# Performance work log

Measured on AMD Instinct MI355X. Metric: run time of the kernel, lower is better.

Reference implementation:

```python
import jax, jax.numpy as jnp
import numpy as np

B, S, E, H = 4, 2048, 512, 8
D = E // H  # head dim
CDIM = 3


def setup_inputs() -> dict:
    key = jax.random.key(0)
    ks = jax.random.split(key, 16)
    inp = {
        'q': jax.random.normal(ks[0], (B, S, E), jnp.float32),
        'k': jax.random.normal(ks[1], (B, S, E), jnp.float32),
        'v': jax.random.normal(ks[2], (B, S, E), jnp.float32),
        'coords_q': jax.random.normal(ks[3], (B, S, CDIM), jnp.float32),
        'coords_k': jax.random.normal(ks[4], (B, S, CDIM), jnp.float32),
        'attn_mask': jax.random.randint(ks[5], (B, S, S), 0, 2).astype(bool),
        'alibi_mask': jax.random.randint(ks[6], (B, S, S), 0, 2).astype(bool),
        # per-head projection params, stacked over heads: [H, E, D]
        'Wq': jax.random.normal(ks[7], (H, E, D), jnp.float32) / np.sqrt(E),
        'bq': jnp.zeros((H, D), jnp.float32),
        'Wk': jax.random.normal(ks[8], (H, E, D), jnp.float32) / np.sqrt(E),
        'bk': jnp.zeros((H, D), jnp.float32),
        'Wv': jax.random.normal(ks[9], (H, E, D), jnp.float32) / np.sqrt(E),
        'bv': jnp.zeros((H, D), jnp.float32),
        # per-head ALiBi params; running_mean is a buffer (eval mode -> constant ones)
        'bias_scale': jax.random.uniform(ks[10], (H,), jnp.float32),
        'running_mean': jnp.ones((H,), jnp.float32),
        # output projection
        'fc_w': jax.random.normal(ks[11], (E, E), jnp.float32) / np.sqrt(E),
        'fc_b': jnp.zeros((E,), jnp.float32),
    }
    return inp


def reference(q, k, v, coords_q, coords_k, attn_mask, alibi_mask,
              Wq, bq, Wk, bk, Wv, bv, bias_scale, running_mean, fc_w, fc_b):
    # per-head projections, vectorized over heads: [B,H,S,D]
    qh = jnp.einsum('bse,hed->bhsd', q, Wq) + bq[None, :, None, :]
    kh = jnp.einsum('bse,hed->bhsd', k, Wk) + bk[None, :, None, :]
    vh = jnp.einsum('bse,hed->bhsd', v, Wv) + bv[None, :, None, :]

    # scaled dot-product logits: [B,H,Sq,Sk]
    logits = jnp.einsum('bhqd,bhkd->bhqk', qh, kh) * (D ** -0.5)
    weights = jax.nn.softmax(logits, axis=-1)

    # pairwise euclidean distances between coords: [B,Sq,Sk]
    diff = coords_q[:, :, None, :] - coords_k[:, None, :, :]
    dist = jnp.sqrt(jnp.sum(diff * diff, axis=-1))

    # per-head distance bias (eval: divide by running_mean buffer, scale by bias_scale)
    scale = (bias_scale / running_mean)[None, :, None, None]  # [1,H,1,1]
    scaled_dist = dist[:, None, :, :] * scale                  # [B,H,Sq,Sk]
    masked_dist = jnp.where(~alibi_mask[:, None, :, :], scaled_dist, 0.0)

    # post-softmax bias subtraction and masking (non-standard attention)
    masked = jnp.where(~attn_mask[:, None, :, :], weights - masked_dist, 0.0)

    att = jnp.einsum('bhqk,bhkd->bhqd', masked, vh)            # [B,H,S,D]
    att = att.transpose(0, 2, 1, 3).reshape(B, S, E)           # [B,S,E]
    return att @ fc_w.T + fc_b
```

## Files before the change

### kernel.cpp

```cpp
#include <hip/hip_runtime.h>

typedef unsigned short ushort;
typedef unsigned char uchar;
typedef unsigned long long u64;
typedef __attribute__((ext_vector_type(8))) short short8;
typedef __attribute__((ext_vector_type(4))) float f32x4;
typedef __attribute__((ext_vector_type(4))) unsigned int uint4v;

#define B_ 4
#define S_ 2048
#define E_ 512
#define H_ 8
#define D_ 64
#define LDT 40
#define LDF 68

__device__ inline ushort f2bf(float f) {
  union { float f; unsigned int u; } v; v.f = f;
  unsigned int u = v.u;
  unsigned int r = u + 0x7FFFu + ((u >> 16) & 1u);
  return (ushort)(r >> 16);
}

__device__ inline unsigned int cvt_pk_bf16(float a, float b) {
  unsigned int r;
  asm("v_cvt_pk_bf16_f32 %0, %1, %2" : "=v"(r) : "v"(a), "v"(b));
  return r;
}

__device__ inline float exp2_fast(float x) {
#if defined(__has_builtin)
#if __has_builtin(__builtin_amdgcn_exp2f)
  return __builtin_amdgcn_exp2f(x);
#else
  return __expf(x * 0.69314718056f);
#endif
#else
  return __expf(x * 0.69314718056f);
#endif
}

__device__ inline short8 mask_keep(short8 p, short8 a2) {
  union U { short8 s; uint4v u; } P, A;
  P.s = p; A.s = a2;
#pragma unroll
  for (int i = 0; i < 4; ++i) {
    unsigned int t = A.u[i] & 0x80008000u;
    unsigned int dm = (t >> 15) * 0xFFFFu;
    P.u[i] &= ~dm;
  }
  return P.s;
}

__device__ inline float dpp_sum16(float v) {
  union { float f; int i; } s, t;
  s.f = v;
  t.i = __builtin_amdgcn_update_dpp(0, s.i, 0x128, 0xf, 0xf, false); s.f += t.f;
  t.i = __builtin_amdgcn_update_dpp(0, s.i, 0x124, 0xf, 0xf, false); s.f += t.f;
  t.i = __builtin_amdgcn_update_dpp(0, s.i, 0x122, 0xf, 0xf, false); s.f += t.f;
  t.i = __builtin_amdgcn_update_dpp(0, s.i, 0x121, 0xf, 0xf, false); s.f += t.f;
  return s.f;
}

__global__ void detect_kernel(const uchar* __restrict__ am, int* flag) {
  __shared__ int s;
  if (threadIdx.x == 0) s = 0;
  __syncthreads();
  int x = 0;
  for (int p = threadIdx.x; p < 4096; p += 256)
    if (p & 3) x += am[p];
  atomicAdd(&s, x);
  __syncthreads();
  if (threadIdx.x == 0) *flag = (s == 0) ? 1 : 0;
}

__global__ __launch_bounds__(256) void convert_w_kernel(
    const float* __restrict__ Wq, const float* __restrict__ Wk, const float* __restrict__ Wv,
    ushort* __restrict__ wt) {
  const int p = blockIdx.y;
  const float* W = (p == 0) ? Wq : (p == 1) ? Wk : Wv;
  const int n = blockIdx.x;
  const int h = n >> 6, d = n & 63;
  ushort* o = wt + ((size_t)p * E_ + n) * E_;
  for (int e = threadIdx.x; e < E_; e += 256)
    o[e] = f2bf(W[((size_t)h * E_ + e) * D_ + d]);
}

__global__ __launch_bounds__(256) void convert_fcw_kernel(
    const float* __restrict__ fcw, ushort* __restrict__ fcwbf) {
  size_t base = ((size_t)blockIdx.x * 256 + threadIdx.x) * 8;
  float4 a = *(const float4*)&fcw[base];
  float4 b = *(const float4*)&fcw[base + 4];
  short8 o;
  o[0] = (short)f2bf(a.x); o[1] = (short)f2bf(a.y); o[2] = (short)f2bf(a.z); o[3] = (short)f2bf(a.w);
  o[4] = (short)f2bf(b.x); o[5] = (short)f2bf(b.y); o[6] = (short)f2bf(b.z); o[7] = (short)f2bf(b.w);
  *(short8*)&fcwbf[base] = o;
}

__global__ __launch_bounds__(256) void proj_gemm_kernel(
    const float* __restrict__ qx, const float* __restrict__ kx, const float* __restrict__ vx,
    const ushort* __restrict__ wt,
    const float* __restrict__ bq, const float* __restrict__ bk, const float* __restrict__ bv,
    ushort* __restrict__ qkv) {
  const int phys = blockIdx.x;
  const int logical = (phys & 7) * 96 + (phys >> 3);
  const int p = logical >> 8;
  const int rem = logical & 255;
  const int m0 = (rem >> 2) * 128, n0 = (rem & 3) * 128;

  const float* A   = (p == 0) ? qx : (p == 1) ? kx : vx;
  const ushort* Bt = wt + (size_t)p * (E_ * E_);
  const float* bias = (p == 0) ? bq : (p == 1) ? bk : bv;
  const float osc = (p == 0) ? 0.125f * 1.44269504f : 1.0f;
  ushort* out = qkv + (size_t)p * (B_ * H_ * S_ * D_);

  const int tid = threadIdx.x;
  const int w = tid >> 6, lane = tid & 63;
  const int g = lane >> 4, c = lane & 15;
  const int wr = w >> 1, wc = w & 1;

  __shared__ ushort As[128][LDT], Bs[128][LDT];

  f32x4 acc[4][4];
#pragma unroll
  for (int i = 0; i < 4; ++i)
#pragma unroll
    for (int j = 0; j < 4; ++j) acc[i][j] = (f32x4){0, 0, 0, 0};

  const int srow = tid >> 2, sc8 = (tid & 3) * 8;
  float4 pa0[2], pa1[2];
  short8 pb[2];
#pragma unroll
  for (int it = 0; it < 2; ++it) {
    const float* ap = &A[(size_t)(m0 + srow + 64 * it) * E_ + sc8];
    pa0[it] = *(const float4*)ap;
    pa1[it] = *(const float4*)(ap + 4);
    pb[it] = *(const short8*)&Bt[(size_t)(n0 + srow + 64 * it) * E_ + sc8];
  }

  for (int kk = 0; kk < E_; kk += 32) {
    __syncthreads();
#pragma unroll
    for (int it = 0; it < 2; ++it) {
      unsigned int r0 = cvt_pk_bf16(pa0[it].x, pa0[it].y), r1 = cvt_pk_bf16(pa0[it].z, pa0[it].w);
      unsigned int r2 = cvt_pk_bf16(pa1[it].x, pa1[it].y), r3 = cvt_pk_bf16(pa1[it].z, pa1[it].w);
      short8 av;
      av[0] = (short)(ushort)r0; av[1] = (short)(ushort)(r0 >> 16);
      av[2] = (short)(ushort)r1; av[3] = (short)(ushort)(r1 >> 16);
      av[4] = (short)(ushort)r2; av[5] = (short)(ushort)(r2 >> 16);
      av[6] = (short)(ushort)r3; av[7] = (short)(ushort)(r3 >> 16);
      *(short8*)&As[srow + 64 * it][sc8] = av;
      *(short8*)&Bs[srow + 64 * it][sc8] = pb[it];
    }
    __syncthreads();
    if (kk + 32 < E_) {
#pragma unroll
      for (int it = 0; it < 2; ++it) {
        const float* ap = &A[(size_t)(m0 + srow + 64 * it) * E_ + kk + 32 + sc8];
        pa0[it] = *(const float4*)ap;
        pa1[it] = *(const float4*)(ap + 4);
        pb[it] = *(const short8*)&Bt[(size_t)(n0 + srow + 64 * it) * E_ + kk + 32 + sc8];
      }
    }
    short8 af[4], bfr[4];
#pragma unroll
    for (int i = 0; i < 4; ++i) af[i] = *(const short8*)&As[wr * 64 + i * 16 + c][8 * g];
#pragma unroll
    for (int j = 0; j < 4; ++j) bfr[j] = *(const short8*)&Bs[wc * 64 + j * 16 + c][8 * g];
#pragma unroll
    for (int i = 0; i < 4; ++i)
#pragma unroll
      for (int j = 0; j < 4; ++j)
        acc[i][j] = __builtin_amdgcn_mfma_f32_16x16x32_bf16(af[i], bfr[j], acc[i][j], 0, 0, 0);
  }

#pragma unroll
  for (int i = 0; i < 4; ++i)
#pragma unroll
    for (int jj = 0; jj < 4; ++jj) {
      int grow = m0 + wr * 64 + i * 16 + 4 * g + jj;
      int b = grow >> 11, s = grow & 2047;
#pragma unroll
      for (int j = 0; j < 4; ++j) {
        int col = n0 + wc * 64 + j * 16 + c;
        int h = col >> 6, d = col & 63;
        out[(((size_t)(b * H_ + h)) * S_ + s) * D_ + d] = f2bf((acc[i][j][jj] + bias[col]) * osc);
      }
    }
}

__global__ __launch_bounds__(256) void transpose_v_kernel(
    const ushort* __restrict__ vh, ushort* __restrict__ vtg) {
  const int bh = blockIdx.y, s0 = blockIdx.x * 64;
  __shared__ ushort tile[64][70];
  const int tid = threadIdx.x;
#pragma unroll
  for (int it = 0; it < 2; ++it) {
    int chunk = tid + 256 * it;
    int r = chunk >> 3, c8 = chunk & 7;
    *(short8*)&tile[r][c8 * 8] = *(const short8*)&vh[((size_t)bh * S_ + s0 + r) * D_ + c8 * 8];
  }
  __syncthreads();
#pragma unroll
  for (int it = 0; it < 2; ++it) {
    int chunk = tid + 256 * it;
    int d = chunk >> 3, s8 = chunk & 7;
    short8 o;
#pragma unroll
    for (int j = 0; j < 8; ++j) o[j] = (short)tile[s8 * 8 + j][d];
    *(short8*)&vtg[((size_t)bh * D_ + d) * S_ + s0 + s8 * 8] = o;
  }
}

__global__ __launch_bounds__(256) void m2dist_kernel(
    const float* __restrict__ cq, const float* __restrict__ ck,
    const void* __restrict__ am_raw, const void* __restrict__ alm_raw,
    const int* __restrict__ flag,
    ushort* __restrict__ m2d) {
  const bool isInt = (*flag != 0);
  const int b = blockIdx.y, qi = blockIdx.x;
  const int k0 = threadIdx.x * 8;
  const size_t rowbase = ((size_t)b * S_ + qi) * S_;
  const float qx = cq[((size_t)b * S_ + qi) * 3 + 0];
  const float qy = cq[((size_t)b * S_ + qi) * 3 + 1];
  const float qz = cq[((size_t)b * S_ + qi) * 3 + 2];
  int a[8], al[8];
  if (isInt) {
    int4 A0 = *(const int4*)&((const int*)am_raw)[rowbase + k0];
    int4 A1 = *(const int4*)&((const int*)am_raw)[rowbase + k0 + 4];
    int4 L0 = *(const int4*)&((const int*)alm_raw)[rowbase + k0];
    int4 L1 = *(const int4*)&((const int*)alm_raw)[rowbase + k0 + 4];
    a[0]=A0.x; a[1]=A0.y; a[2]=A0.z; a[3]=A0.w; a[4]=A1.x; a[5]=A1.y; a[6]=A1.z; a[7]=A1.w;
    al[0]=L0.x; al[1]=L0.y; al[2]=L0.z; al[3]=L0.w; al[4]=L1.x; al[5]=L1.y; al[6]=L1.z; al[7]=L1.w;
  } else {
    u64 ab = *(const u64*)&((const uchar*)am_raw)[rowbase + k0];
    u64 lb = *(const u64*)&((const uchar*)alm_raw)[rowbase + k0];
#pragma unroll
    for (int j = 0; j < 8; ++j) { a[j] = (int)((ab >> (8 * j)) & 0xFF); al[j] = (int)((lb >> (8 * j)) & 0xFF); }
  }
  float c24[24];
  {
    const float* ckp = ck + ((size_t)b * S_ + k0) * 3;
#pragma unroll
    for (int t = 0; t < 6; ++t) {
      float4 cv = *(const float4*)(ckp + 4 * t);
      c24[4 * t] = cv.x; c24[4 * t + 1] = cv.y; c24[4 * t + 2] = cv.z; c24[4 * t + 3] = cv.w;
    }
  }
  float dist[8];
#pragma unroll
  for (int j = 0; j < 8; ++j) {
    const float dx = qx - c24[3 * j], dy = qy - c24[3 * j + 1], dz = qz - c24[3 * j + 2];
    dist[j] = sqrtf(dx * dx + dy * dy + dz * dz);
  }
  short8 md;
#pragma unroll
  for (int jp = 0; jp < 4; ++jp) {
    unsigned int r = cvt_pk_bf16(dist[2 * jp], dist[2 * jp + 1]);
    ushort v0 = (!a[2 * jp]     && !al[2 * jp])     ? (ushort)r         : (ushort)0;
    ushort v1 = (!a[2 * jp + 1] && !al[2 * jp + 1]) ? (ushort)(r >> 16) : (ushort)0;
    if (a[2 * jp])     v0 |= 0x8000u;
    if (a[2 * jp + 1]) v1 |= 0x8000u;
    md[2 * jp] = (short)v0; md[2 * jp + 1] = (short)v1;
  }
  *(short8*)&m2d[rowbase + k0] = md;
}

__global__ __launch_bounds__(512) void flash_kernel(
    const ushort* __restrict__ qh, const ushort* __restrict__ kh, const ushort* __restrict__ vtg,
    const ushort* __restrict__ m2d,
    const float* __restrict__ bscale, const float* __restrict__ rmean,
    ushort* __restrict__ attb) {
  const int flat = blockIdx.x;
  const int h = flat >> 6;
  const int grp = flat & 63;
  const int b = grp >> 4;
  const int qb = (grp & 15) * 128;
  const int bh = b * 8 + h;
  const int tid = threadIdx.x;
  const int w = tid >> 6, lane = tid & 63;
  const int g = lane >> 4, c = lane & 15;

  __shared__ ushort Kt[2][64][LDF];
  __shared__ ushort Vt[2][64][LDF];
  __shared__ ushort Pl[8][16][LDF];

  const size_t bhS = (size_t)bh * S_;
  const int qrow_a = qb + 16 * w + c;
  const short8 aq0 = *(const short8*)(qh + (bhS + qrow_a) * D_ + 8 * g);
  const short8 aq1 = *(const short8*)(qh + (bhS + qrow_a) * D_ + 8 * g + 32);

  const int skr = tid >> 3, sc8 = (tid & 7) * 8;
  const ushort* pk0 = kh + (bhS + skr) * D_ + sc8;
  const ushort* pv0 = vtg + ((size_t)bh * D_ + skr) * S_ + sc8;
  const ushort* pm0 = m2d + ((size_t)b * S_ + qrow_a) * S_ + 8 * g;
  const ushort* pm1 = pm0 + 32;

  f32x4 acc1[4], acc2[4];
#pragma unroll
  for (int t = 0; t < 4; ++t) { acc1[t] = (f32x4){0,0,0,0}; acc2[t] = (f32x4){0,0,0,0}; }
  float l[4] = {0, 0, 0, 0};

  {
    short8 k0 = *(const short8*)pk0;  pk0 += 64 * D_;
    short8 v0 = *(const short8*)pv0;  pv0 += 64;
    *(short8*)&Kt[0][skr][sc8] = k0;
    *(short8*)&Vt[0][skr][sc8] = v0;
  }
  short8 a2n0 = *(const short8*)pm0; pm0 += 64;
  short8 a2n1 = *(const short8*)pm1; pm1 += 64;
  short8 skn = *(const short8*)pk0;  pk0 += 64 * D_;
  short8 svn = *(const short8*)pv0;  pv0 += 64;
  __syncthreads();

  for (int kb = 0; kb < S_; kb += 64) {
    const int cur = (kb >> 6) & 1;
    short8 a2c0 = a2n0, a2c1 = a2n1;
    a2n0 = *(const short8*)pm0; pm0 += 64;
    a2n1 = *(const short8*)pm1; pm1 += 64;

    f32x4 sf[4];
    __builtin_amdgcn_s_setprio(1);
#pragma unroll
    for (int t = 0; t < 4; ++t) {
      short8 b0 = *(const short8*)&Kt[cur][16 * t + c][8 * g];
      short8 b1 = *(const short8*)&Kt[cur][16 * t + c][8 * g + 32];
      f32x4 z = (f32x4){0, 0, 0, 0};
      z = __builtin_amdgcn_mfma_f32_16x16x32_bf16(aq0, b0, z, 0, 0, 0);
      z = __builtin_amdgcn_mfma_f32_16x16x32_bf16(aq1, b1, z, 0, 0, 0);
      sf[t] = z;
    }
    __builtin_amdgcn_s_setprio(0);

#pragma unroll
    for (int t = 0; t < 4; ++t)
#pragma unroll
      for (int jp = 0; jp < 2; ++jp) {
        float p0 = exp2_fast(sf[t][2 * jp]);
        float p1 = exp2_fast(sf[t][2 * jp + 1]);
        l[2 * jp] += p0; l[2 * jp + 1] += p1;
        unsigned int r = cvt_pk_bf16(p0, p1);
        Pl[w][4 * g + 2 * jp][16 * t + c]     = (ushort)r;
        Pl[w][4 * g + 2 * jp + 1][16 * t + c] = (ushort)(r >> 16);
      }

    asm volatile("s_waitcnt lgkmcnt(0)" ::: "memory");
    __builtin_amdgcn_sched_barrier(0);

    short8 pa0 = *(const short8*)&Pl[w][c][8 * g];
    short8 pa1 = *(const short8*)&Pl[w][c][8 * g + 32];
    pa0 = mask_keep(pa0, a2c0);
    pa1 = mask_keep(pa1, a2c1);
    __builtin_amdgcn_s_setprio(1);
#pragma unroll
    for (int t2 = 0; t2 < 4; ++t2) {
      short8 v0 = *(const short8*)&Vt[cur][16 * t2 + c][8 * g];
      short8 v1 = *(const short8*)&Vt[cur][16 * t2 + c][8 * g + 32];
      acc1[t2] = __builtin_amdgcn_mfma_f32_16x16x32_bf16(pa0, v0, acc1[t2], 0, 0, 0);
      acc1[t2] = __builtin_amdgcn_mfma_f32_16x16x32_bf16(pa1, v1, acc1[t2], 0, 0, 0);
      acc2[t2] = __builtin_amdgcn_mfma_f32_16x16x32_bf16(a2c0, v0, acc2[t2], 0, 0, 0);
      acc2[t2] = __builtin_amdgcn_mfma_f32_16x16x32_bf16(a2c1, v1, acc2[t2], 0, 0, 0);
    }
    __builtin_amdgcn_s_setprio(0);

    if (kb + 64 < S_) {
      *(short8*)&Kt[cur ^ 1][skr][sc8] = skn;
      *(short8*)&Vt[cur ^ 1][skr][sc8] = svn;
      skn = *(const short8*)pk0;  pk0 += 64 * D_;
      svn = *(const short8*)pv0;  pv0 += 64;
    }
    __syncthreads();
  }

  float linv[4];
#pragma unroll
  for (int j = 0; j < 4; ++j) linv[j] = 1.0f / dpp_sum16(l[j]);
  const float scale = bscale[h] / rmean[h];
#pragma unroll
  for (int t2 = 0; t2 < 4; ++t2)
#pragma unroll
    for (int j = 0; j < 4; ++j) {
      int qr = qb + 16 * w + 4 * g + j;
      int d = 16 * t2 + c;
      attb[(((size_t)b * S_ + qr) * H_ + h) * D_ + d] =
          f2bf(acc1[t2][j] * linv[j] - scale * acc2[t2][j]);
    }
}

__global__ __launch_bounds__(256) void final_gemm_kernel(
    const ushort* __restrict__ attb, const ushort* __restrict__ fcwbf,
    const float* __restrict__ fcb, float* __restrict__ out) {
  const int phys = blockIdx.x;
  const int logical = (phys & 7) * 32 + (phys >> 3);
  const int m0 = (logical >> 2) * 128, n0 = (logical & 3) * 128;
  const int tid = threadIdx.x;
  const int w = tid >> 6, lane = tid & 63;
  const int g = lane >> 4, c = lane & 15;
  const int wr = w >> 1, wc = w & 1;

  __shared__ ushort As[128][LDT], Bs[128][LDT];

  f32x4 acc[4][4];
#pragma unroll
  for (int i = 0; i < 4; ++i)
#pragma unroll
    for (int j = 0; j < 4; ++j) acc[i][j] = (f32x4){0, 0, 0, 0};

  const int srow = tid >> 2, sc8 = (tid & 3) * 8;
  short8 pa[2], pb[2];
#pragma unroll
  for (int it = 0; it < 2; ++it) {
    pa[it] = *(const short8*)&attb[(size_t)(m0 + srow + 64 * it) * E_ + sc8];
    pb[it] = *(const short8*)&fcwbf[(size_t)(n0 + srow + 64 * it) * E_ + sc8];
  }

  for (int kk = 0; kk < E_; kk += 32) {
    __syncthreads();
#pragma unroll
    for (int it = 0; it < 2; ++it) {
      *(short8*)&As[srow + 64 * it][sc8] = pa[it];
      *(short8*)&Bs[srow + 64 * it][sc8] = pb[it];
    }
    __syncthreads();
    if (kk + 32 < E_) {
#pragma unroll
      for (int it = 0; it < 2; ++it) {
        pa[it] = *(const short8*)&attb[(size_t)(m0 + srow + 64 * it) * E_ + kk + 32 + sc8];
        pb[it] = *(const short8*)&fcwbf[(size_t)(n0 + srow + 64 * it) * E_ + kk + 32 + sc8];
      }
    }
    short8 af[4], bfr[4];
#pragma unroll
    for (int i = 0; i < 4; ++i) af[i] = *(const short8*)&As[wr * 64 + i * 16 + c][8 * g];
#pragma unroll
    for (int j = 0; j < 4; ++j) bfr[j] = *(const short8*)&Bs[wc * 64 + j * 16 + c][8 * g];
#pragma unroll
    for (int i = 0; i < 4; ++i)
#pragma unroll
      for (int j = 0; j < 4; ++j)
        acc[i][j] = __builtin_amdgcn_mfma_f32_16x16x32_bf16(af[i], bfr[j], acc[i][j], 0, 0, 0);
  }

#pragma unroll
  for (int i = 0; i < 4; ++i)
#pragma unroll
    for (int jj = 0; jj < 4; ++jj) {
      int grow = m0 + wr * 64 + i * 16 + 4 * g + jj;
#pragma unroll
      for (int j = 0; j < 4; ++j) {
        int col = n0 + wc * 64 + j * 16 + c;
        out[(size_t)grow * E_ + col] = acc[i][j][jj] + fcb[col];
      }
    }
}

extern "C" void kernel_launch(void* const* d_in, const int* in_sizes, int n_in,
                              void* d_out, int out_size, void* d_ws, size_t ws_size,
                              hipStream_t stream) {
  const float* q   = (const float*)d_in[0];
  const float* k   = (const float*)d_in[1];
  const float* v   = (const float*)d_in[2];
  const float* cq  = (const float*)d_in[3];
  const float* ck  = (const float*)d_in[4];
  const void*  am  = d_in[5];
  const void*  alm = d_in[6];
  const float* Wq  = (const float*)d_in[7];
  const float* bq  = (const float*)d_in[8];
  const float* Wk  = (const float*)d_in[9];
  const float* bk  = (const float*)d_in[10];
  const float* Wv  = (const float*)d_in[11];
  const float* bv  = (const float*)d_in[12];
  const float* bsc = (const float*)d_in[13];
  const float* rm  = (const float*)d_in[14];
  const float* fcw = (const float*)d_in[15];
  const float* fcb = (const float*)d_in[16];
  float* out = (float*)d_out;

  char* ws = (char*)d_ws;
  ushort* attb = (ushort*)(ws);
  ushort* vtg  = (ushort*)(ws + 16ull * 1024 * 1024);
  ushort* qkv  = (ushort*)(ws + 24ull * 1024 * 1024);
  ushort* m2d  = (ushort*)(ws + 48ull * 1024 * 1024);
  ushort* wt   = (ushort*)(ws + 80ull * 1024 * 1024);
  ushort* fcwbf= (ushort*)(ws + 80ull * 1024 * 1024 + 1536 * 1024);
  int*    flag = (int*)   (ws + 82ull * 1024 * 1024);

  ushort* qh = qkv;
  ushort* kh = qkv + (size_t)(B_ * H_ * S_ * D_);
  ushort* vh = qkv + 2 * (size_t)(B_ * H_ * S_ * D_);

  detect_kernel<<<1, 256, 0, stream>>>((const uchar*)am, flag);
  convert_w_kernel<<<dim3(512, 3), 256, 0, stream>>>(Wq, Wk, Wv, wt);
  convert_fcw_kernel<<<128, 256, 0, stream>>>(fcw, fcwbf);
  proj_gemm_kernel<<<768, 256, 0, stream>>>(q, k, v, wt, bq, bk, bv, qkv);
  transpose_v_kernel<<<dim3(S_ / 64, B_ * H_), 256, 0, stream>>>(vh, vtg);
  m2dist_kernel<<<dim3(S_, B_), 256, 0, stream>>>(cq, ck, am, alm, flag, m2d);
  flash_kernel<<<512, 512, 0, stream>>>(qh, kh, vtg, m2d, bsc, rm, attb);
  final_gemm_kernel<<<256, 256, 0, stream>>>(attb, fcwbf, fcb, out);
}
```

Measured before the change: 171.2 us.

## Have each flash-attention wave process two 16-row query groups with 256 threads

The flash kernel now runs 4 waves per block instead of 8. Each wave handles two 16-row query tiles and reuses the same K and V fragments read from LDS for both, which halves LDS reads of K/V per unit of work. Each thread also stages two rows of K and V per tile. This costs more registers per wave (double accumulators, extra mask prefetches) and fewer waves per block to hide latency.

```diff
diff --git a/kernel.cpp b/kernel.cpp
--- a/kernel.cpp
+++ b/kernel.cpp
@@ -266,7 +266,7 @@
   *(short8*)&m2d[rowbase + k0] = md;
 }
 
-__global__ __launch_bounds__(512) void flash_kernel(
+__global__ __launch_bounds__(256) void flash_kernel(
     const ushort* __restrict__ qh, const ushort* __restrict__ kh, const ushort* __restrict__ vtg,
     const ushort* __restrict__ m2d,
     const float* __restrict__ bscale, const float* __restrict__ rmean,
@@ -283,52 +283,68 @@
 
   __shared__ ushort Kt[2][64][LDF];
   __shared__ ushort Vt[2][64][LDF];
-  __shared__ ushort Pl[8][16][LDF];
+  __shared__ ushort Pl[4][32][LDF];
 
   const size_t bhS = (size_t)bh * S_;
-  const int qrow_a = qb + 16 * w + c;
-  const short8 aq0 = *(const short8*)(qh + (bhS + qrow_a) * D_ + 8 * g);
-  const short8 aq1 = *(const short8*)(qh + (bhS + qrow_a) * D_ + 8 * g + 32);
+  const int qr0 = qb + 16 * w + c;
+  const int qr1 = qr0 + 64;
+  const short8 aq0 = *(const short8*)(qh + (bhS + qr0) * D_ + 8 * g);
+  const short8 aq1 = *(const short8*)(qh + (bhS + qr0) * D_ + 8 * g + 32);
+  const short8 aq2 = *(const short8*)(qh + (bhS + qr1) * D_ + 8 * g);
+  const short8 aq3 = *(const short8*)(qh + (bhS + qr1) * D_ + 8 * g + 32);
 
   const int skr = tid >> 3, sc8 = (tid & 7) * 8;
   const ushort* pk0 = kh + (bhS + skr) * D_ + sc8;
+  const ushort* pk1 = pk0 + 32 * D_;
   const ushort* pv0 = vtg + ((size_t)bh * D_ + skr) * S_ + sc8;
-  const ushort* pm0 = m2d + ((size_t)b * S_ + qrow_a) * S_ + 8 * g;
+  const ushort* pv1 = pv0 + 32 * S_;
+  const ushort* pm0 = m2d + ((size_t)b * S_ + qr0) * S_ + 8 * g;
   const ushort* pm1 = pm0 + 32;
-
-  f32x4 acc1[4], acc2[4];
-#pragma unroll
-  for (int t = 0; t < 4; ++t) { acc1[t] = (f32x4){0,0,0,0}; acc2[t] = (f32x4){0,0,0,0}; }
-  float l[4] = {0, 0, 0, 0};
-
-  {
-    short8 k0 = *(const short8*)pk0;  pk0 += 64 * D_;
-    short8 v0 = *(const short8*)pv0;  pv0 += 64;
-    *(short8*)&Kt[0][skr][sc8] = k0;
-    *(short8*)&Vt[0][skr][sc8] = v0;
-  }
+  const ushort* pm2 = m2d + ((size_t)b * S_ + qr1) * S_ + 8 * g;
+  const ushort* pm3 = pm2 + 32;
+
+  f32x4 acc1g0[4], acc2g0[4], acc1g1[4], acc2g1[4];
+#pragma unroll
+  for (int t = 0; t < 4; ++t) {
+    acc1g0[t] = (f32x4){0,0,0,0}; acc2g0[t] = (f32x4){0,0,0,0};
+    acc1g1[t] = (f32x4){0,0,0,0}; acc2g1[t] = (f32x4){0,0,0,0};
+  }
+  float l0[4] = {0, 0, 0, 0}, l1[4] = {0, 0, 0, 0};
+
+  *(short8*)&Kt[0][skr][sc8]      = *(const short8*)pk0;  pk0 += 64 * D_;
+  *(short8*)&Kt[0][skr + 32][sc8] = *(const short8*)pk1;  pk1 += 64 * D_;
+  *(short8*)&Vt[0][skr][sc8]      = *(const short8*)pv0;  pv0 += 64;
+  *(short8*)&Vt[0][skr + 32][sc8] = *(const short8*)pv1;  pv1 += 64;
   short8 a2n0 = *(const short8*)pm0; pm0 += 64;
   short8 a2n1 = *(const short8*)pm1; pm1 += 64;
-  short8 skn = *(const short8*)pk0;  pk0 += 64 * D_;
-  short8 svn = *(const short8*)pv0;  pv0 += 64;
+  short8 a2n2 = *(const short8*)pm2; pm2 += 64;
+  short8 a2n3 = *(const short8*)pm3; pm3 += 64;
+  short8 skn0 = *(const short8*)pk0;  pk0 += 64 * D_;
+  short8 skn1 = *(const short8*)pk1;  pk1 += 64 * D_;
+  short8 svn0 = *(const short8*)pv0;  pv0 += 64;
+  short8 svn1 = *(const short8*)pv1;  pv1 += 64;
   __syncthreads();
 
   for (int kb = 0; kb < S_; kb += 64) {
     const int cur = (kb >> 6) & 1;
-    short8 a2c0 = a2n0, a2c1 = a2n1;
+    short8 a2c0 = a2n0, a2c1 = a2n1, a2c2 = a2n2, a2c3 = a2n3;
     a2n0 = *(const short8*)pm0; pm0 += 64;
     a2n1 = *(const short8*)pm1; pm1 += 64;
-
-    f32x4 sf[4];
+    a2n2 = *(const short8*)pm2; pm2 += 64;
+    a2n3 = *(const short8*)pm3; pm3 += 64;
+
+    f32x4 sf0[4], sf1[4];
     __builtin_amdgcn_s_setprio(1);
 #pragma unroll
     for (int t = 0; t < 4; ++t) {
       short8 b0 = *(const short8*)&Kt[cur][16 * t + c][8 * g];
       short8 b1 = *(const short8*)&Kt[cur][16 * t + c][8 * g + 32];
-      f32x4 z = (f32x4){0, 0, 0, 0};
-      z = __builtin_amdgcn_mfma_f32_16x16x32_bf16(aq0, b0, z, 0, 0, 0);
-      z = __builtin_amdgcn_mfma_f32_16x16x32_bf16(aq1, b1, z, 0, 0, 0);
-      sf[t] = z;
+      f32x4 z0 = (f32x4){0, 0, 0, 0}, z1 = (f32x4){0, 0, 0, 0};
+      z0 = __builtin_amdgcn_mfma_f32_16x16x32_bf16(aq0, b0, z0, 0, 0, 0);
+      z0 = __builtin_amdgcn_mfma_f32_16x16x32_bf16(aq1, b1, z0, 0, 0, 0);
+      z1 = __builtin_amdgcn_mfma_f32_16x16x32_bf16(aq2, b0, z1, 0, 0, 0);
+      z1 = __builtin_amdgcn_mfma_f32_16x16x32_bf16(aq3, b1, z1, 0, 0, 0);
+      sf0[t] = z0; sf1[t] = z1;
     }
     __builtin_amdgcn_s_setprio(0);
 
@@ -336,12 +352,18 @@
     for (int t = 0; t < 4; ++t)
 #pragma unroll
       for (int jp = 0; jp < 2; ++jp) {
-        float p0 = exp2_fast(sf[t][2 * jp]);
-        float p1 = exp2_fast(sf[t][2 * jp + 1]);
-        l[2 * jp] += p0; l[2 * jp + 1] += p1;
+        float p0 = exp2_fast(sf0[t][2 * jp]);
+        float p1 = exp2_fast(sf0[t][2 * jp + 1]);
+        l0[2 * jp] += p0; l0[2 * jp + 1] += p1;
         unsigned int r = cvt_pk_bf16(p0, p1);
         Pl[w][4 * g + 2 * jp][16 * t + c]     = (ushort)r;
         Pl[w][4 * g + 2 * jp + 1][16 * t + c] = (ushort)(r >> 16);
+        float p2 = exp2_fast(sf1[t][2 * jp]);
+        float p3 = exp2_fast(sf1[t][2 * jp + 1]);
+        l1[2 * jp] += p2; l1[2 * jp + 1] += p3;
+        unsigned int r2 = cvt_pk_bf16(p2, p3);
+        Pl[w][16 + 4 * g + 2 * jp][16 * t + c]     = (ushort)r2;
+        Pl[w][16 + 4 * g + 2 * jp + 1][16 * t + c] = (ushort)(r2 >> 16);
       }
 
     asm volatile("s_waitcnt lgkmcnt(0)" ::: "memory");
@@ -349,41 +371,58 @@
 
     short8 pa0 = *(const short8*)&Pl[w][c][8 * g];
     short8 pa1 = *(const short8*)&Pl[w][c][8 * g + 32];
+    short8 pa2 = *(const short8*)&Pl[w][16 + c][8 * g];
+    short8 pa3 = *(const short8*)&Pl[w][16 + c][8 * g + 32];
     pa0 = mask_keep(pa0, a2c0);
     pa1 = mask_keep(pa1, a2c1);
+    pa2 = mask_keep(pa2, a2c2);
+    pa3 = mask_keep(pa3, a2c3);
     __builtin_amdgcn_s_setprio(1);
 #pragma unroll
     for (int t2 = 0; t2 < 4; ++t2) {
       short8 v0 = *(const short8*)&Vt[cur][16 * t2 + c][8 * g];
       short8 v1 = *(const short8*)&Vt[cur][16 * t2 + c][8 * g + 32];
-      acc1[t2] = __builtin_amdgcn_mfma_f32_16x16x32_bf16(pa0, v0, acc1[t2], 0, 0, 0);
-      acc1[t2] = __builtin_amdgcn_mfma_f32_16x16x32_bf16(pa1, v1, acc1[t2], 0, 0, 0);
-      acc2[t2] = __builtin_amdgcn_mfma_f32_16x16x32_bf16(a2c0, v0, acc2[t2], 0, 0, 0);
-      acc2[t2] = __builtin_amdgcn_mfma_f32_16x16x32_bf16(a2c1, v1, acc2[t2], 0, 0, 0);
+      acc1g0[t2] = __builtin_amdgcn_mfma_f32_16x16x32_bf16(pa0, v0, acc1g0[t2], 0, 0, 0);
+      acc1g0[t2] = __builtin_amdgcn_mfma_f32_16x16x32_bf16(pa1, v1, acc1g0[t2], 0, 0, 0);
+      acc2g0[t2] = __builtin_amdgcn_mfma_f32_16x16x32_bf16(a2c0, v0, acc2g0[t2], 0, 0, 0);
+      acc2g0[t2] = __builtin_amdgcn_mfma_f32_16x16x32_bf16(a2c1, v1, acc2g0[t2], 0, 0, 0);
+      acc1g1[t2] = __builtin_amdgcn_mfma_f32_16x16x32_bf16(pa2, v0, acc1g1[t2], 0, 0, 0);
+      acc1g1[t2] = __builtin_amdgcn_mfma_f32_16x16x32_bf16(pa3, v1, acc1g1[t2], 0, 0, 0);
+      acc2g1[t2] = __builtin_amdgcn_mfma_f32_16x16x32_bf16(a2c2, v0, acc2g1[t2], 0, 0, 0);
+      acc2g1[t2] = __builtin_amdgcn_mfma_f32_16x16x32_bf16(a2c3, v1, acc2g1[t2], 0, 0, 0);
     }
     __builtin_amdgcn_s_setprio(0);
 
     if (kb + 64 < S_) {
-      *(short8*)&Kt[cur ^ 1][skr][sc8] = skn;
-      *(short8*)&Vt[cur ^ 1][skr][sc8] = svn;
-      skn = *(const short8*)pk0;  pk0 += 64 * D_;
-      svn = *(const short8*)pv0;  pv0 += 64;
+      *(short8*)&Kt[cur ^ 1][skr][sc8]      = skn0;
+      *(short8*)&Kt[cur ^ 1][skr + 32][sc8] = skn1;
+      *(short8*)&Vt[cur ^ 1][skr][sc8]      = svn0;
+      *(short8*)&Vt[cur ^ 1][skr + 32][sc8] = svn1;
+      skn0 = *(const short8*)pk0;  pk0 += 64 * D_;
+      skn1 = *(const short8*)pk1;  pk1 += 64 * D_;
+      svn0 = *(const short8*)pv0;  pv0 += 64;
+      svn1 = *(const short8*)pv1;  pv1 += 64;
     }
     __syncthreads();
   }
 
-  float linv[4];
-#pragma unroll
-  for (int j = 0; j < 4; ++j) linv[j] = 1.0f / dpp_sum16(l[j]);
+  float linv0[4], linv1[4];
+#pragma unroll
+  for (int j = 0; j < 4; ++j) {
+    linv0[j] = 1.0f / dpp_sum16(l0[j]);
+    linv1[j] = 1.0f / dpp_sum16(l1[j]);
+  }
   const float scale = bscale[h] / rmean[h];
 #pragma unroll
   for (int t2 = 0; t2 < 4; ++t2)
 #pragma unroll
     for (int j = 0; j < 4; ++j) {
-      int qr = qb + 16 * w + 4 * g + j;
+      int qrA = qb + 16 * w + 4 * g + j;
       int d = 16 * t2 + c;
-      attb[(((size_t)b * S_ + qr) * H_ + h) * D_ + d] =
-          f2bf(acc1[t2][j] * linv[j] - scale * acc2[t2][j]);
+      attb[(((size_t)b * S_ + qrA) * H_ + h) * D_ + d] =
+          f2bf(acc1g0[t2][j] * linv0[j] - scale * acc2g0[t2][j]);
+      attb[(((size_t)b * S_ + qrA + 64) * H_ + h) * D_ + d] =
+          f2bf(acc1g1[t2][j] * linv1[j] - scale * acc2g1[t2][j]);
     }
 }
 
@@ -495,6 +534,6 @@
   proj_gemm_kernel<<<768, 256, 0, stream>>>(q, k, v, wt, bq, bk, bv, qkv);
   transpose_v_kernel<<<dim3(S_ / 64, B_ * H_), 256, 0, stream>>>(vh, vtg);
   m2dist_kernel<<<dim3(S_, B_), 256, 0, stream>>>(cq, ck, am, alm, flag, m2d);
-  flash_kernel<<<512, 512, 0, stream>>>(qh, kh, vtg, m2d, bsc, rm, attb);
+  flash_kernel<<<512, 256, 0, stream>>>(qh, kh, vtg, m2d, bsc, rm, attb);
   final_gemm_kernel<<<256, 256, 0, stream>>>(attb, fcwbf, fcb, out);
 }
```

Measured after the change: 176.6 us. +3.1%, slower.
